# Performance work log

Hardware: AMD Instinct MI355X
Metric: run time of the kernel (lower is better)

## Reference

```python
import jax, jax.numpy as jnp
import numpy as np

# dims
B, T = 128, 1024
INP, HUMAN = 54, 64          # input_dim, output_dim (HUMAN_SIZE)
DEC, ENC = 256, 256          # decoder / encoder GRU sizes
K, H_PSI, LR_PSI = 16, 256, 32
N_PSI = DEC*DEC + DEC + DEC*INP + DEC*HUMAN + INP*(HUMAN-INP)  # 96540


def setup_inputs() -> dict:
    key = jax.random.key(0)
    ks = jax.random.split(key, 16)
    g = lambda i, shape, s=0.05: jax.random.normal(ks[i], shape, jnp.float32) * s
    return {
        "inputs": g(0, (B, T, INP), 1.0),
        "state": jnp.zeros((B, DEC), jnp.float32),
        "eps": g(1, (B, K), 1.0),
        # encoder GRUCell params (torch gate order r,z,n)
        "enc_Wih": g(2, (3*ENC, INP)),
        "enc_Whh": g(3, (3*ENC, ENC)),
        "enc_bih": jnp.zeros((3*ENC,), jnp.float32),
        "enc_bhh": jnp.zeros((3*ENC,), jnp.float32),
        # latent projections
        "to_mu": g(4, (K, ENC)),
        "to_lsigma": g(5, (K, ENC)),
        # psi hypernetwork MLP
        "W1": g(6, (H_PSI, K)),   "b1": jnp.zeros((H_PSI,), jnp.float32),
        "W2": g(7, (LR_PSI, H_PSI)), "b2": jnp.zeros((LR_PSI,), jnp.float32),
        "W3": g(8, (N_PSI, LR_PSI), 0.01), "b3": jnp.zeros((N_PSI,), jnp.float32),
        # shared decoder gate params (bias second half init to ones, as in module)
        "gru_Wih": g(9, (2*DEC, INP)),
        "gru_Whh": g(10, (DEC, 2*DEC)),
        "gru_bias": jnp.concatenate([jnp.zeros((DEC,)), jnp.ones((DEC,))]).astype(jnp.float32),
    }


def reference(inputs, state, eps, enc_Wih, enc_Whh, enc_bih, enc_bhh,
              to_mu, to_lsigma, W1, b1, W2, b2, W3, b3,
              gru_Wih, gru_Whh, gru_bias):
    x_tbd = jnp.swapaxes(inputs, 0, 1)  # [T,B,INP]

    # ---- encoder GRU scan (torch GRUCell semantics) ----
    def enc_step(h, x_t):
        gi = x_t @ enc_Wih.T + enc_bih
        gh = h @ enc_Whh.T + enc_bhh
        ir, iz, inn = jnp.split(gi, 3, axis=-1)
        hr, hz, hn = jnp.split(gh, 3, axis=-1)
        r = jax.nn.sigmoid(ir + hr)
        z = jax.nn.sigmoid(iz + hz)
        n = jnp.tanh(inn + r * hn)
        return (1 - z) * n + z * h, None

    h_enc, _ = jax.lax.scan(enc_step, jnp.zeros((inputs.shape[0], ENC), inputs.dtype), x_tbd)

    # ---- MT latent ----
    mu = h_enc @ to_mu.T                 # [B,K]
    logstd = h_enc @ to_lsigma.T         # [B,K]
    z_lat = mu + eps * jnp.exp(logstd)

    # ---- psi hypernetwork ----
    psi = jnp.tanh(z_lat @ W1.T + b1) @ W2.T + b2
    psi = psi @ W3.T + b3                # [B, N_PSI]

    o = 0
    Whh_p = psi[:, o:o+DEC*DEC].reshape(-1, DEC, DEC); o += DEC*DEC
    bh_p  = psi[:, o:o+DEC];                           o += DEC
    Wih_p = psi[:, o:o+DEC*INP].reshape(-1, DEC, INP); o += DEC*INP
    C_p   = psi[:, o:o+DEC*HUMAN].reshape(-1, DEC, HUMAN); o += DEC*HUMAN
    D_p   = psi[:, o:o+INP*(HUMAN-INP)].reshape(-1, INP, HUMAN-INP)

    # ---- per-sample hypernet-weighted GRU decoder, vectorized over batch ----
    def dec_step(h, x_t):  # h:[B,DEC], x_t:[B,INP]
        gx = x_t @ gru_Wih.T                       # [B,2*DEC]
        gh = h @ gru_Whh                           # [B,2*DEC]
        zt = jax.nn.sigmoid(gx[:, :DEC] + gh[:, :DEC] + gru_bias[:DEC])
        rt = jax.nn.sigmoid(gx[:, DEC:] + gh[:, DEC:] + gru_bias[DEC:])
        eta = jnp.tanh(jnp.einsum('bd,bhd->bh', x_t, Wih_p)
                       + rt * jnp.tanh(jnp.einsum('bh,bhg->bg', h, Whh_p) + bh_p))
        h_new = zt * h + (1 - zt) * eta
        return h_new, h_new

    h_last, dec_seq = jax.lax.scan(dec_step, state, x_tbd)
    dec_seq = jnp.swapaxes(dec_seq, 0, 1)          # [B,T,DEC]

    # yhat = dec@C + cat(zeros, x@D) ; residual adds inputs to first INP cols
    yD = jnp.einsum('btd,bde->bte', inputs, D_p)   # [B,T,HUMAN-INP]
    yhats = jnp.einsum('bth,bho->bto', dec_seq, C_p) + jnp.concatenate([inputs, yD], axis=-1)

    return yhats, mu, logstd, h_last
```

## Files before the change

### kernel.cpp

```cpp
#include <hip/hip_runtime.h>

#define BB 128
#define TT 1024
#define INP 54
#define HUM 64
#define NPSI 96540
#define OFF_BH 65536
#define OFF_WIH 65792
#define OFF_C 79616
#define OFF_D 96000
#define OUT_MU 8388608
#define OUT_LS 8390656
#define OUT_HL 8392704

typedef unsigned int u32;
typedef unsigned short u16;
typedef _Float16 h2 __attribute__((ext_vector_type(2)));

__device__ __forceinline__ u32 pk(float a, float b) {
    h2 v; v.x = (_Float16)a; v.y = (_Float16)b;
    return __builtin_bit_cast(u32, v);
}
__device__ __forceinline__ float f16tof(u16 v) {
    return (float)__builtin_bit_cast(_Float16, v);
}
__device__ __forceinline__ u16 ftof16(float v) {
    return __builtin_bit_cast(u16, (_Float16)v);
}
__device__ __forceinline__ float lo16f(u32 v) { return f16tof((u16)(v & 0xffffu)); }
__device__ __forceinline__ float hi16f(u32 v) { return f16tof((u16)(v >> 16)); }
__device__ __forceinline__ h2 bch2(u32 a) { return __builtin_bit_cast(h2, a); }
__device__ __forceinline__ float fd2(u32 a, u32 b, float c) {
#if __has_builtin(__builtin_amdgcn_fdot2)
    return __builtin_amdgcn_fdot2(bch2(a), bch2(b), c, false);
#else
    return c + lo16f(a) * lo16f(b) + hi16f(a) * hi16f(b);
#endif
}
__device__ __forceinline__ float fsig(float x) { return 1.f / (1.f + __expf(-x)); }
__device__ __forceinline__ float ftanh(float x) { float e = __expf(2.f * x); return 1.f - 2.f / (e + 1.f); }

__device__ __forceinline__ float qred(float v) {
#if __has_builtin(__builtin_amdgcn_mov_dpp)
    int x = __builtin_bit_cast(int, v);
    v += __builtin_bit_cast(float, __builtin_amdgcn_mov_dpp(x, 0xB1, 0xF, 0xF, true));
    x = __builtin_bit_cast(int, v);
    v += __builtin_bit_cast(float, __builtin_amdgcn_mov_dpp(x, 0x4E, 0xF, 0xF, true));
    return v;
#else
    v += __shfl_xor(v, 1); v += __shfl_xor(v, 2);
    return v;
#endif
}

__global__ __launch_bounds__(768, 3) void gemm_x_kernel(
    const float* __restrict__ inp, const float* __restrict__ W0,
    const u16* __restrict__ psi16, int mode, int t0, int len, int ct, int nt,
    u16* __restrict__ gout)
{
    const int tid = threadIdx.x;
    const int b = blockIdx.x / nt, tc = blockIdx.x % nt;
    const int gr = tid;
    float w[INP];
    if (mode == 0 || gr < 512) {
        const float* wsrc = W0 + (size_t)gr * INP;
#pragma unroll
        for (int c = 0; c < INP; ++c) w[c] = wsrc[c];
    } else {
        const u16* wsrc = psi16 + (size_t)b * NPSI + OFF_WIH + (size_t)(gr - 512) * INP;
#pragma unroll
        for (int c = 0; c < INP; ++c) w[c] = f16tof(wsrc[c]);
    }
    const int tb = tc * 128;
    const int te = (tb + 128 < len) ? tb + 128 : len;
    for (int tl = tb; tl < te; ++tl) {
        const float* xr = inp + ((size_t)b * TT + t0 + tl) * INP;
        float a = 0.f;
#pragma unroll
        for (int c = 0; c < INP; ++c) a = __builtin_fmaf(xr[c], w[c], a);
        gout[((size_t)b * ct + tl) * 768 + gr] = ftof16(a);
    }
}

__global__ __launch_bounds__(512) __attribute__((amdgpu_waves_per_eu(2, 2)))
void enc_scan_kernel(
    const u16* __restrict__ gi, int t0, int len, int ct,
    const float* __restrict__ Whh, const float* __restrict__ bih,
    const float* __restrict__ bhh, float* __restrict__ hcarry)
{
    __shared__ __align__(16) u32 hpp[2][144];
    const int tid = threadIdx.x, b = blockIdx.x;
    const int l = tid & 3, g = tid >> 2;
    const int j0 = 2 * g, j1 = 2 * g + 1;

    u32 wr0[32], wz0[32], wn0[32], wr1[32], wz1[32], wn1[32];
    {
        const float* pr0 = Whh + (size_t)j0 * 256 + 64 * l;
        const float* pz0 = Whh + (size_t)(256 + j0) * 256 + 64 * l;
        const float* pn0 = Whh + (size_t)(512 + j0) * 256 + 64 * l;
        const float* pr1 = Whh + (size_t)j1 * 256 + 64 * l;
        const float* pz1 = Whh + (size_t)(256 + j1) * 256 + 64 * l;
        const float* pn1 = Whh + (size_t)(512 + j1) * 256 + 64 * l;
#pragma unroll
        for (int c = 0; c < 32; ++c) {
            wr0[c] = pk(pr0[2 * c], pr0[2 * c + 1]);
            wz0[c] = pk(pz0[2 * c], pz0[2 * c + 1]);
            wn0[c] = pk(pn0[2 * c], pn0[2 * c + 1]);
            wr1[c] = pk(pr1[2 * c], pr1[2 * c + 1]);
            wz1[c] = pk(pz1[2 * c], pz1[2 * c + 1]);
            wn1[c] = pk(pn1[2 * c], pn1[2 * c + 1]);
        }
    }
    const float brb0 = bih[j0] + bhh[j0],             brb1 = bih[j1] + bhh[j1];
    const float bzb0 = bih[256 + j0] + bhh[256 + j0], bzb1 = bih[256 + j1] + bhh[256 + j1];
    const float bib0 = bih[512 + j0],                 bib1 = bih[512 + j1];
    const float bhb0 = bhh[512 + j0],                 bhb1 = bhh[512 + j1];
    float hc0 = 0.f, hc1 = 0.f;
    if (t0 > 0) { hc0 = hcarry[(size_t)b * 256 + j0]; hc1 = hcarry[(size_t)b * 256 + j1]; }
    if (tid < 128) {
        u32 hv = 0u;
        if (t0 > 0) hv = pk(hcarry[(size_t)b * 256 + 2 * tid], hcarry[(size_t)b * 256 + 2 * tid + 1]);
        hpp[0][36 * (tid >> 5) + (tid & 31)] = hv;
    }
    __syncthreads();

    const u16* gbase = gi + (size_t)b * ct * 768;
    u32 c0 = *(const u32*)(gbase + 2 * g);
    u32 c1 = *(const u32*)(gbase + 256 + 2 * g);
    u32 c2 = *(const u32*)(gbase + 512 + 2 * g);

    for (int tl = 0; tl < len; ++tl) {
        const int p = tl & 1;
        u32 n0 = 0, n1 = 0, n2 = 0;
        if (tl + 1 < len) {
            const u16* gn = gbase + (size_t)(tl + 1) * 768;
            n0 = *(const u32*)(gn + 2 * g);
            n1 = *(const u32*)(gn + 256 + 2 * g);
            n2 = *(const u32*)(gn + 512 + 2 * g);
        }
        float ar0 = 0, az0 = 0, ah0 = 0, ar1 = 0, az1 = 0, ah1 = 0;
        const uint4* hq = (const uint4*)hpp[p];
#pragma unroll
        for (int cc = 0; cc < 8; ++cc) {
            uint4 q = hq[9 * l + cc];
            u32 qa[4] = {q.x, q.y, q.z, q.w};
#pragma unroll
            for (int u = 0; u < 4; ++u) {
                const int c = cc * 4 + u;
                ar0 = fd2(wr0[c], qa[u], ar0);
                az0 = fd2(wz0[c], qa[u], az0);
                ah0 = fd2(wn0[c], qa[u], ah0);
                ar1 = fd2(wr1[c], qa[u], ar1);
                az1 = fd2(wz1[c], qa[u], az1);
                ah1 = fd2(wn1[c], qa[u], ah1);
            }
        }
        ar0 = qred(ar0); az0 = qred(az0); ah0 = qred(ah0);
        ar1 = qred(ar1); az1 = qred(az1); ah1 = qred(ah1);
        {
            float r0 = fsig(ar0 + lo16f(c0) + brb0);
            float z0 = fsig(az0 + lo16f(c1) + bzb0);
            float nn0 = ftanh(lo16f(c2) + bib0 + r0 * (ah0 + bhb0));
            float hn0 = (1.f - z0) * nn0 + z0 * hc0;
            float r1 = fsig(ar1 + hi16f(c0) + brb1);
            float z1 = fsig(az1 + hi16f(c1) + bzb1);
            float nn1 = ftanh(hi16f(c2) + bib1 + r1 * (ah1 + bhb1));
            float hn1 = (1.f - z1) * nn1 + z1 * hc1;
            hc0 = hn0; hc1 = hn1;
            if (l == 0) hpp[p ^ 1][36 * (g >> 5) + (g & 31)] = pk(hn0, hn1);
        }
        c0 = n0; c1 = n1; c2 = n2;
        __syncthreads();
    }
    if (l == 0) {
        hcarry[(size_t)b * 256 + j0] = hc0;
        hcarry[(size_t)b * 256 + j1] = hc1;
    }
}

__global__ __launch_bounds__(256) void latent_kernel(
    const float* __restrict__ henc, const float* __restrict__ eps,
    const float* __restrict__ to_mu, const float* __restrict__ to_ls,
    const float* __restrict__ W1, const float* __restrict__ b1,
    const float* __restrict__ W2, const float* __restrict__ b2,
    float* __restrict__ psi2, float* __restrict__ out)
{
    __shared__ float h[256], zz[16], p1[256];
    const int tid = threadIdx.x, b = blockIdx.x;
    h[tid] = henc[(size_t)b * 256 + tid];
    __syncthreads();
    if (tid < 16) {
        float m = 0, s = 0;
        for (int k = 0; k < 256; ++k) {
            m += h[k] * to_mu[tid * 256 + k];
            s += h[k] * to_ls[tid * 256 + k];
        }
        out[OUT_MU + b * 16 + tid] = m;
        out[OUT_LS + b * 16 + tid] = s;
        zz[tid] = m + eps[b * 16 + tid] * __expf(s);
    }
    __syncthreads();
    {
        float a = b1[tid];
        for (int k = 0; k < 16; ++k) a += zz[k] * W1[tid * 16 + k];
        p1[tid] = ftanh(a);
    }
    __syncthreads();
    if (tid < 32) {
        float a = b2[tid];
        for (int k = 0; k < 256; ++k) a += p1[k] * W2[tid * 256 + k];
        psi2[b * 32 + tid] = a;
    }
}

__global__ __launch_bounds__(256) void psi3_kernel(
    const float* __restrict__ psi2, const float* __restrict__ W3,
    const float* __restrict__ b3, u16* __restrict__ psi16)
{
    __shared__ float sp2[128 * 32];
    __shared__ float w3t[256 * 33];
    const int tid = threadIdx.x;
    const int n0 = blockIdx.x * 256;
    for (int idx = tid; idx < 4096; idx += 256) sp2[idx] = psi2[idx];
    for (int idx = tid; idx < 8192; idx += 256) {
        int row = idx >> 5, k = idx & 31;
        int n = n0 + row;
        w3t[row * 33 + k] = (n < NPSI) ? W3[(size_t)n * 32 + k] : 0.f;
    }
    __syncthreads();
    const int n = n0 + tid;
    if (n < NPSI) {
        float w[32];
#pragma unroll
        for (int k = 0; k < 32; ++k) w[k] = w3t[tid * 33 + k];
        const float bv = b3[n];
        for (int bi = 0; bi < 128; ++bi) {
            float a = bv;
#pragma unroll
            for (int k = 0; k < 32; ++k) a += sp2[bi * 32 + k] * w[k];
            psi16[(size_t)bi * NPSI + n] = ftof16(a);
        }
    }
}

__global__ __launch_bounds__(512) __attribute__((amdgpu_waves_per_eu(2, 2)))
void dec_scan_kernel(
    const u16* __restrict__ gx, int t0, int len, int ct,
    const float* __restrict__ state, const float* __restrict__ gWhh,
    const float* __restrict__ gbias, const u16* __restrict__ psi16,
    float* __restrict__ dcarry, u32* __restrict__ hseq, float* __restrict__ out)
{
    __shared__ __align__(16) u32 hpp[2][144];
    __shared__ __align__(16) u32 gxs32[2][3072];
    const int tid = threadIdx.x, b = blockIdx.x;
    const int l = tid & 3, g = tid >> 2;
    const int j0 = 2 * g, j1 = 2 * g + 1;
    const u16* pc = psi16 + (size_t)b * NPSI;

    u32 wz0[32], wr0[32], wp0[32], wz1[32], wr1[32], wp1[32];
#pragma unroll
    for (int c = 0; c < 32; ++c) {
        const int h0 = 64 * l + 2 * c;
        wz0[c] = pk(gWhh[(size_t)h0 * 512 + j0], gWhh[(size_t)(h0 + 1) * 512 + j0]);
        wr0[c] = pk(gWhh[(size_t)h0 * 512 + 256 + j0], gWhh[(size_t)(h0 + 1) * 512 + 256 + j0]);
        wp0[c] = (u32)pc[(size_t)h0 * 256 + j0] | ((u32)pc[(size_t)(h0 + 1) * 256 + j0] << 16);
        wz1[c] = pk(gWhh[(size_t)h0 * 512 + j1], gWhh[(size_t)(h0 + 1) * 512 + j1]);
        wr1[c] = pk(gWhh[(size_t)h0 * 512 + 256 + j1], gWhh[(size_t)(h0 + 1) * 512 + 256 + j1]);
        wp1[c] = (u32)pc[(size_t)h0 * 256 + j1] | ((u32)pc[(size_t)(h0 + 1) * 256 + j1] << 16);
    }
    const float gzb0 = gbias[j0], gzb1 = gbias[j1];
    const float grb0 = gbias[256 + j0], grb1 = gbias[256 + j1];
    const float bhb0 = f16tof(pc[OFF_BH + j0]), bhb1 = f16tof(pc[OFF_BH + j1]);
    const float* hsrc = (t0 == 0) ? state : dcarry;
    float hc0 = hsrc[(size_t)b * 256 + j0];
    float hc1 = hsrc[(size_t)b * 256 + j1];
    if (tid < 128) hpp[0][36 * (tid >> 5) + (tid & 31)] =
        pk(hsrc[(size_t)b * 256 + 2 * tid], hsrc[(size_t)b * 256 + 2 * tid + 1]);
    const u32* gb32 = (const u32*)(gx + (size_t)b * ct * 768);
    {
        const int steps0 = (len < 8) ? len : 8;
#pragma unroll
        for (int k = 0; k < 6; ++k) {
            const int f = k * 512 + tid;
            if (f < 384 * steps0) gxs32[0][f] = gb32[f];
        }
    }
    __syncthreads();

    u32* hsb = hseq + (size_t)b * TT * 128;
    int buf = 0;
    for (int cb = 0; cb < len; cb += 8) {
        const int steps = (len - cb < 8) ? (len - cb) : 8;
        const int nsteps = (len - cb - 8 < 8) ? (len - cb - 8) : 8;
        u32 stg[6];
        if (nsteps > 0) {
            const u32* gsrc = gb32 + (size_t)(cb + 8) * 384;
#pragma unroll
            for (int k = 0; k < 6; ++k) {
                const int f = k * 512 + tid;
                if (f < 384 * nsteps) stg[k] = gsrc[f];
            }
        }
        for (int st = 0; st < steps; ++st) {
            const int tl = cb + st;
            const int p = tl & 1;
            const u16* gx16 = (const u16*)gxs32[buf];
            const u32 c0 = *(const u32*)(gx16 + st * 768 + 2 * g);
            const u32 c1 = *(const u32*)(gx16 + st * 768 + 256 + 2 * g);
            const u32 c2 = *(const u32*)(gx16 + st * 768 + 512 + 2 * g);
            float az0 = 0, ar0 = 0, ap0 = 0, az1 = 0, ar1 = 0, ap1 = 0;
            const uint4* hq = (const uint4*)hpp[p];
#pragma unroll
            for (int cc = 0; cc < 8; ++cc) {
                uint4 q = hq[9 * l + cc];
                u32 qa[4] = {q.x, q.y, q.z, q.w};
#pragma unroll
                for (int u = 0; u < 4; ++u) {
                    const int c = cc * 4 + u;
                    az0 = fd2(wz0[c], qa[u], az0);
                    ar0 = fd2(wr0[c], qa[u], ar0);
                    ap0 = fd2(wp0[c], qa[u], ap0);
                    az1 = fd2(wz1[c], qa[u], az1);
                    ar1 = fd2(wr1[c], qa[u], ar1);
                    ap1 = fd2(wp1[c], qa[u], ap1);
                }
            }
            az0 = qred(az0); ar0 = qred(ar0); ap0 = qred(ap0);
            az1 = qred(az1); ar1 = qred(ar1); ap1 = qred(ap1);
            {
                float zt0 = fsig(az0 + lo16f(c0) + gzb0);
                float rt0 = fsig(ar0 + lo16f(c1) + grb0);
                float eta0 = ftanh(lo16f(c2) + rt0 * ftanh(ap0 + bhb0));
                float hn0 = zt0 * hc0 + (1.f - zt0) * eta0;
                float zt1 = fsig(az1 + hi16f(c0) + gzb1);
                float rt1 = fsig(ar1 + hi16f(c1) + grb1);
                float eta1 = ftanh(hi16f(c2) + rt1 * ftanh(ap1 + bhb1));
                float hn1 = zt1 * hc1 + (1.f - zt1) * eta1;
                hc0 = hn0; hc1 = hn1;
                if (l == 0) {
                    u32 hv = pk(hn0, hn1);
                    hpp[p ^ 1][36 * (g >> 5) + (g & 31)] = hv;
                    hsb[(size_t)(t0 + tl) * 128 + g] = hv;
                }
            }
            __syncthreads();
        }
        if (nsteps > 0) {
#pragma unroll
            for (int k = 0; k < 6; ++k) {
                const int f = k * 512 + tid;
                if (f < 384 * nsteps) gxs32[buf ^ 1][f] = stg[k];
            }
        }
        __syncthreads();
        buf ^= 1;
    }
    if (l == 0) {
        dcarry[(size_t)b * 256 + j0] = hc0;
        dcarry[(size_t)b * 256 + j1] = hc1;
        if (t0 + len == TT) {
            out[OUT_HL + (size_t)b * 256 + j0] = hc0;
            out[OUT_HL + (size_t)b * 256 + j1] = hc1;
        }
    }
}

#define YT 32
__global__ __launch_bounds__(256) void yhat_kernel(
    const u32* __restrict__ hseq, const u16* __restrict__ psi16,
    float* __restrict__ out)
{
    __shared__ float part[2][YT][64];
    const int tid = threadIdx.x;
    const int b = blockIdx.x >> 5, tile = blockIdx.x & 31;
    const int o = tid & 63, s = (tid >> 6) & 1, tq = tid >> 7;
    const u16* pc = psi16 + (size_t)b * NPSI;
    u32 cpr[64];
#pragma unroll
    for (int i = 0; i < 64; ++i) {
        const int gp = s * 64 + i;
        cpr[i] = (u32)pc[OFF_C + (size_t)(2 * gp) * 64 + o]
               | ((u32)pc[OFF_C + (size_t)(2 * gp + 1) * 64 + o] << 16);
    }
    const int t0 = tile * YT;
    for (int th = 0; th < YT / 2; ++th) {
        const int tl = tq * (YT / 2) + th;
        const uint4* h4 = (const uint4*)(hseq + ((size_t)b * TT + t0 + tl) * 128 + s * 64);
        float a = 0.f;
#pragma unroll
        for (int gc = 0; gc < 16; ++gc) {
            uint4 q = h4[gc];
            a = fd2(q.x, cpr[gc * 4 + 0], a);
            a = fd2(q.y, cpr[gc * 4 + 1], a);
            a = fd2(q.z, cpr[gc * 4 + 2], a);
            a = fd2(q.w, cpr[gc * 4 + 3], a);
        }
        part[s][tl][o] = a;
    }
    __syncthreads();
    for (int i = 0; i < 8; ++i) {
        const int flat = i * 256 + tid;
        const int tl = flat >> 6, o2 = flat & 63;
        out[((size_t)b * TT + t0 + tl) * HUM + o2] = part[0][tl][o2] + part[1][tl][o2];
    }
}

__global__ __launch_bounds__(256) void post_kernel(
    const float* __restrict__ inp, const u16* __restrict__ psi16,
    float* __restrict__ out)
{
    __shared__ float xs[128][55];
    __shared__ float ds[INP][10];
    const int tid = threadIdx.x;
    const int b = blockIdx.x >> 3, tile = blockIdx.x & 7;
    const int t0 = tile * 128;
    const u16* pc = psi16 + (size_t)b * NPSI;
    for (int idx = tid; idx < 540; idx += 256)
        ds[idx / 10][idx % 10] = f16tof(pc[OFF_D + idx]);
    for (int idx = tid; idx < 128 * INP; idx += 256) {
        const int t = idx / INP, d = idx % INP;
        xs[t][d] = inp[((size_t)b * TT + t0 + t) * INP + d];
    }
    __syncthreads();
    for (int i = 0; i < 32; ++i) {
        const int flat = i * 256 + tid;
        const int t = flat >> 6, o = flat & 63;
        const size_t oi = ((size_t)b * TT + t0 + t) * HUM + o;
        float y = out[oi];
        if (o < INP) y += xs[t][o];
        else {
            float acc = 0.f;
            for (int d = 0; d < INP; ++d) acc += xs[t][d] * ds[d][o - INP];
            y += acc;
        }
        out[oi] = y;
    }
}

extern "C" void kernel_launch(void* const* d_in, const int* in_sizes, int n_in,
                              void* d_out, int out_size, void* d_ws, size_t ws_size,
                              hipStream_t stream)
{
    const float* inputs = (const float*)d_in[0];
    const float* state  = (const float*)d_in[1];
    const float* eps    = (const float*)d_in[2];
    const float* eWih   = (const float*)d_in[3];
    const float* eWhh   = (const float*)d_in[4];
    const float* ebih   = (const float*)d_in[5];
    const float* ebhh   = (const float*)d_in[6];
    const float* to_mu  = (const float*)d_in[7];
    const float* to_ls  = (const float*)d_in[8];
    const float* W1     = (const float*)d_in[9];
    const float* b1     = (const float*)d_in[10];
    const float* W2     = (const float*)d_in[11];
    const float* b2     = (const float*)d_in[12];
    const float* W3     = (const float*)d_in[13];
    const float* b3     = (const float*)d_in[14];
    const float* gWih   = (const float*)d_in[15];
    const float* gWhh   = (const float*)d_in[16];
    const float* gbias  = (const float*)d_in[17];
    float* out = (float*)d_out;
    float* ws  = (float*)d_ws;

    float* henc   = ws;
    float* psi2   = ws + 32768;
    float* dcarry = ws + 36864;
    u16*   psi16  = (u16*)(ws + 69632);
    u32*   hseq   = (u32*)(ws + 6248192);
    u16*   gbuf   = (u16*)(ws + 23025408);
    const size_t used = (size_t)23025408 * 4;
    size_t avail = (ws_size > used + 4096) ? (ws_size - used - 4096) : 0;
    int ct = (int)(avail / ((size_t)BB * 768 * 2));
    if (ct > TT) ct = TT;
    if (ct < 1) ct = 1;

    for (int t0 = 0; t0 < TT; t0 += ct) {
        const int len = (TT - t0 < ct) ? (TT - t0) : ct;
        const int nt = (len + 127) / 128;
        gemm_x_kernel<<<BB * nt, 768, 0, stream>>>(inputs, eWih, psi16, 0, t0, len, ct, nt, gbuf);
        enc_scan_kernel<<<BB, 512, 0, stream>>>(gbuf, t0, len, ct, eWhh, ebih, ebhh, henc);
    }
    latent_kernel<<<BB, 256, 0, stream>>>(henc, eps, to_mu, to_ls, W1, b1, W2, b2, psi2, out);
    psi3_kernel<<<(NPSI + 255) / 256, 256, 0, stream>>>(psi2, W3, b3, psi16);
    for (int t0 = 0; t0 < TT; t0 += ct) {
        const int len = (TT - t0 < ct) ? (TT - t0) : ct;
        const int nt = (len + 127) / 128;
        gemm_x_kernel<<<BB * nt, 768, 0, stream>>>(inputs, gWih, psi16, 1, t0, len, ct, nt, gbuf);
        dec_scan_kernel<<<BB, 512, 0, stream>>>(gbuf, t0, len, ct, state, gWhh, gbias, psi16,
                                                dcarry, hseq, out);
    }
    yhat_kernel<<<BB * 32, 256, 0, stream>>>(hseq, psi16, out);
    post_kernel<<<BB * 8, 256, 0, stream>>>(inputs, psi16, out);
}
```

Baseline: 4.531 ms.

## Fuse post pass into yhat, pack two rows per gemm thread, pin scan VGPRs

The residual/D-projection post kernel is folded into yhat_kernel, so the output tensor is written once instead of being written, re-read and rewritten. gemm_x_kernel now computes two adjacent gate rows per thread with 384 threads, reusing each input load and storing packed half2 words. The scan kernels swap the waves_per_eu hint for an explicit 256-VGPR budget. Together these cut global traffic and launches, but the register attribute may change occupancy or spilling in the latency-bound scans.

```diff
diff --git a/kernel.cpp b/kernel.cpp
--- a/kernel.cpp
+++ b/kernel.cpp
@@ -17,6 +17,12 @@
 typedef unsigned short u16;
 typedef _Float16 h2 __attribute__((ext_vector_type(2)));
 
+#if __has_attribute(amdgpu_num_vgpr)
+#define NUMVGPR256 __attribute__((amdgpu_num_vgpr(256)))
+#else
+#define NUMVGPR256
+#endif
+
 __device__ __forceinline__ u32 pk(float a, float b) {
     h2 v; v.x = (_Float16)a; v.y = (_Float16)b;
     return __builtin_bit_cast(u32, v);
@@ -53,36 +59,42 @@
 #endif
 }
 
-__global__ __launch_bounds__(768, 3) void gemm_x_kernel(
+__global__ __launch_bounds__(384, 2) void gemm_x_kernel(
     const float* __restrict__ inp, const float* __restrict__ W0,
     const u16* __restrict__ psi16, int mode, int t0, int len, int ct, int nt,
     u16* __restrict__ gout)
 {
     const int tid = threadIdx.x;
     const int b = blockIdx.x / nt, tc = blockIdx.x % nt;
-    const int gr = tid;
-    float w[INP];
-    if (mode == 0 || gr < 512) {
-        const float* wsrc = W0 + (size_t)gr * INP;
-#pragma unroll
-        for (int c = 0; c < INP; ++c) w[c] = wsrc[c];
+    const int r0 = 2 * tid, r1 = 2 * tid + 1;
+    float w0[INP], w1[INP];
+    if (mode == 0 || r0 < 512) {
+        const float* s0 = W0 + (size_t)r0 * INP;
+        const float* s1 = W0 + (size_t)r1 * INP;
+#pragma unroll
+        for (int c = 0; c < INP; ++c) { w0[c] = s0[c]; w1[c] = s1[c]; }
     } else {
-        const u16* wsrc = psi16 + (size_t)b * NPSI + OFF_WIH + (size_t)(gr - 512) * INP;
-#pragma unroll
-        for (int c = 0; c < INP; ++c) w[c] = f16tof(wsrc[c]);
+        const u16* s0 = psi16 + (size_t)b * NPSI + OFF_WIH + (size_t)(r0 - 512) * INP;
+        const u16* s1 = psi16 + (size_t)b * NPSI + OFF_WIH + (size_t)(r1 - 512) * INP;
+#pragma unroll
+        for (int c = 0; c < INP; ++c) { w0[c] = f16tof(s0[c]); w1[c] = f16tof(s1[c]); }
     }
     const int tb = tc * 128;
     const int te = (tb + 128 < len) ? tb + 128 : len;
     for (int tl = tb; tl < te; ++tl) {
         const float* xr = inp + ((size_t)b * TT + t0 + tl) * INP;
-        float a = 0.f;
-#pragma unroll
-        for (int c = 0; c < INP; ++c) a = __builtin_fmaf(xr[c], w[c], a);
-        gout[((size_t)b * ct + tl) * 768 + gr] = ftof16(a);
-    }
-}
-
-__global__ __launch_bounds__(512) __attribute__((amdgpu_waves_per_eu(2, 2)))
+        float a0 = 0.f, a1 = 0.f;
+#pragma unroll
+        for (int c = 0; c < INP; ++c) {
+            const float xv = xr[c];
+            a0 = __builtin_fmaf(xv, w0[c], a0);
+            a1 = __builtin_fmaf(xv, w1[c], a1);
+        }
+        *(u32*)(gout + ((size_t)b * ct + tl) * 768 + r0) = pk(a0, a1);
+    }
+}
+
+__global__ __launch_bounds__(512) NUMVGPR256
 void enc_scan_kernel(
     const u16* __restrict__ gi, int t0, int len, int ct,
     const float* __restrict__ Whh, const float* __restrict__ bih,
@@ -243,7 +255,7 @@
     }
 }
 
-__global__ __launch_bounds__(512) __attribute__((amdgpu_waves_per_eu(2, 2)))
+__global__ __launch_bounds__(512) NUMVGPR256
 void dec_scan_kernel(
     const u16* __restrict__ gx, int t0, int len, int ct,
     const float* __restrict__ state, const float* __restrict__ gWhh,
@@ -368,13 +380,16 @@
 #define YT 32
 __global__ __launch_bounds__(256) void yhat_kernel(
     const u32* __restrict__ hseq, const u16* __restrict__ psi16,
-    float* __restrict__ out)
+    const float* __restrict__ inp, float* __restrict__ out)
 {
     __shared__ float part[2][YT][64];
+    __shared__ float xs[YT][55];
+    __shared__ float ds[INP][10];
     const int tid = threadIdx.x;
     const int b = blockIdx.x >> 5, tile = blockIdx.x & 31;
     const int o = tid & 63, s = (tid >> 6) & 1, tq = tid >> 7;
     const u16* pc = psi16 + (size_t)b * NPSI;
+    const int t0 = tile * YT;
     u32 cpr[64];
 #pragma unroll
     for (int i = 0; i < 64; ++i) {
@@ -382,7 +397,12 @@
         cpr[i] = (u32)pc[OFF_C + (size_t)(2 * gp) * 64 + o]
                | ((u32)pc[OFF_C + (size_t)(2 * gp + 1) * 64 + o] << 16);
     }
-    const int t0 = tile * YT;
+    for (int idx = tid; idx < 540; idx += 256)
+        ds[idx / 10][idx % 10] = f16tof(pc[OFF_D + idx]);
+    for (int idx = tid; idx < YT * INP; idx += 256) {
+        const int t = idx / INP, d = idx % INP;
+        xs[t][d] = inp[((size_t)b * TT + t0 + t) * INP + d];
+    }
     for (int th = 0; th < YT / 2; ++th) {
         const int tl = tq * (YT / 2) + th;
         const uint4* h4 = (const uint4*)(hseq + ((size_t)b * TT + t0 + tl) * 128 + s * 64);
@@ -401,39 +421,14 @@
     for (int i = 0; i < 8; ++i) {
         const int flat = i * 256 + tid;
         const int tl = flat >> 6, o2 = flat & 63;
-        out[((size_t)b * TT + t0 + tl) * HUM + o2] = part[0][tl][o2] + part[1][tl][o2];
-    }
-}
-
-__global__ __launch_bounds__(256) void post_kernel(
-    const float* __restrict__ inp, const u16* __restrict__ psi16,
-    float* __restrict__ out)
-{
-    __shared__ float xs[128][55];
-    __shared__ float ds[INP][10];
-    const int tid = threadIdx.x;
-    const int b = blockIdx.x >> 3, tile = blockIdx.x & 7;
-    const int t0 = tile * 128;
-    const u16* pc = psi16 + (size_t)b * NPSI;
-    for (int idx = tid; idx < 540; idx += 256)
-        ds[idx / 10][idx % 10] = f16tof(pc[OFF_D + idx]);
-    for (int idx = tid; idx < 128 * INP; idx += 256) {
-        const int t = idx / INP, d = idx % INP;
-        xs[t][d] = inp[((size_t)b * TT + t0 + t) * INP + d];
-    }
-    __syncthreads();
-    for (int i = 0; i < 32; ++i) {
-        const int flat = i * 256 + tid;
-        const int t = flat >> 6, o = flat & 63;
-        const size_t oi = ((size_t)b * TT + t0 + t) * HUM + o;
-        float y = out[oi];
-        if (o < INP) y += xs[t][o];
+        float y = part[0][tl][o2] + part[1][tl][o2];
+        if (o2 < INP) y += xs[tl][o2];
         else {
             float acc = 0.f;
-            for (int d = 0; d < INP; ++d) acc += xs[t][d] * ds[d][o - INP];
+            for (int d = 0; d < INP; ++d) acc += xs[tl][d] * ds[d][o2 - INP];
             y += acc;
         }
-        out[oi] = y;
+        out[((size_t)b * TT + t0 + tl) * HUM + o2] = y;
     }
 }
 
@@ -477,7 +472,7 @@
     for (int t0 = 0; t0 < TT; t0 += ct) {
         const int len = (TT - t0 < ct) ? (TT - t0) : ct;
         const int nt = (len + 127) / 128;
-        gemm_x_kernel<<<BB * nt, 768, 0, stream>>>(inputs, eWih, psi16, 0, t0, len, ct, nt, gbuf);
+        gemm_x_kernel<<<BB * nt, 384, 0, stream>>>(inputs, eWih, psi16, 0, t0, len, ct, nt, gbuf);
         enc_scan_kernel<<<BB, 512, 0, stream>>>(gbuf, t0, len, ct, eWhh, ebih, ebhh, henc);
     }
     latent_kernel<<<BB, 256, 0, stream>>>(henc, eps, to_mu, to_ls, W1, b1, W2, b2, psi2, out);
@@ -485,10 +480,9 @@
     for (int t0 = 0; t0 < TT; t0 += ct) {
         const int len = (TT - t0 < ct) ? (TT - t0) : ct;
         const int nt = (len + 127) / 128;
-        gemm_x_kernel<<<BB * nt, 768, 0, stream>>>(inputs, gWih, psi16, 1, t0, len, ct, nt, gbuf);
+        gemm_x_kernel<<<BB * nt, 384, 0, stream>>>(inputs, gWih, psi16, 1, t0, len, ct, nt, gbuf);
         dec_scan_kernel<<<BB, 512, 0, stream>>>(gbuf, t0, len, ct, state, gWhh, gbias, psi16,
                                                 dcarry, hseq, out);
     }
-    yhat_kernel<<<BB * 32, 256, 0, stream>>>(hseq, psi16, out);
-    post_kernel<<<BB * 8, 256, 0, stream>>>(inputs, psi16, out);
-}
+    yhat_kernel<<<BB * 32, 256, 0, stream>>>(hseq, psi16, inputs, out);
+}
```

New measurement: 4.603 ms. Within noise of the previous version (+1.6%).
